# Kernel tuning notes

Hardware: AMD Instinct MI355X
Metric: run time of the kernel (lower is better)

The kernel has to match this reference:

```python
import jax, jax.numpy as jnp
import numpy as np
import math

D_MODEL = 64
D_STATE = 16
V_RANGE = 1
K = 3
BATCH, H, W = 4, 32, 32
V_LIST = [(x, y) for x in range(-V_RANGE, V_RANGE + 1) for y in range(-V_RANGE, V_RANGE + 1)]
NUM_V = len(V_LIST)


def _circ_conv(x, w):
    # x: (B, Cin, H, W), w: (Cout, Cin, K, K); circular padding then VALID conv
    p = K // 2
    xp = jnp.pad(x, ((0, 0), (0, 0), (p, p), (p, p)), mode='wrap')
    return jax.lax.conv_general_dilated(
        xp, w, window_strides=(1, 1), padding='VALID',
        dimension_numbers=('NCHW', 'OIHW', 'NCHW'))


def setup_inputs() -> dict:
    key = jax.random.key(0)
    ks = jax.random.split(key, 8)
    fan = 1.0 / math.sqrt(D_MODEL * K * K)
    u_t = jax.random.normal(ks[0], (BATCH, D_MODEL, H, W), dtype=jnp.float32)
    s_prev = jax.random.normal(ks[1], (BATCH, NUM_V, D_MODEL, D_STATE, H, W), dtype=jnp.float32)
    conv_delta_w = jax.random.normal(ks[2], (D_MODEL, D_MODEL, K, K), dtype=jnp.float32) * fan
    conv_delta_b = jax.random.normal(ks[3], (D_MODEL,), dtype=jnp.float32) * 0.01
    conv_B_w = jax.random.normal(ks[4], (D_STATE, D_MODEL, K, K), dtype=jnp.float32) * fan
    conv_C_w = jax.random.normal(ks[5], (D_STATE, D_MODEL, K, K), dtype=jnp.float32) * fan
    log_A_real = jnp.log(0.5 * jnp.ones((D_MODEL, D_STATE), dtype=jnp.float32))
    D = jnp.ones((D_MODEL,), dtype=jnp.float32)
    dt_inv_softplus = jnp.asarray(math.log(math.e - 1.0), dtype=jnp.float32)
    return {
        'u_t': u_t, 's_prev': s_prev,
        'conv_delta_w': conv_delta_w, 'conv_delta_b': conv_delta_b,
        'conv_B_w': conv_B_w, 'conv_C_w': conv_C_w,
        'log_A_real': log_A_real, 'D': D, 'dt_inv_softplus': dt_inv_softplus,
    }


def reference(u_t, s_prev, conv_delta_w, conv_delta_b, conv_B_w, conv_C_w,
              log_A_real, D, dt_inv_softplus):
    # delta: (B, d_model, h, w)
    delta = jax.nn.softplus(_circ_conv(u_t, conv_delta_w)
                            + conv_delta_b[None, :, None, None] + dt_inv_softplus)
    B_val = _circ_conv(u_t, conv_B_w)   # (B, d_state, h, w)
    C_val = _circ_conv(u_t, conv_C_w)   # (B, d_state, h, w)
    A = -jnp.exp(log_A_real)            # (d_model, d_state)
    A_bc = A[None, :, :, None, None]    # (1, d_model, d_state, 1, 1)
    A_bar = jnp.exp(delta[:, :, None] * A_bc)        # (B, d_model, d_state, h, w)
    B_bar = (A_bar - 1.0) / A_bc * B_val[:, None]    # (B, d_model, d_state, h, w)
    u_bc = u_t[:, :, None]              # (B, d_model, 1, h, w)
    C_bc = C_val[:, None]               # (B, 1, d_state, h, w)
    y_skip = u_t * D[None, :, None, None]

    s_next_list, y_list = [], []
    for i, (vx, vy) in enumerate(V_LIST):
        s_tr = jnp.roll(s_prev[:, i], shift=(-vy, -vx), axis=(-2, -1))
        s_new = A_bar * s_tr + B_bar * u_bc          # (B, d_model, d_state, h, w)
        y_new = jnp.sum(s_new * C_bc, axis=2) + y_skip
        s_next_list.append(s_new)
        y_list.append(y_new)
    s_next = jnp.stack(s_next_list, axis=1)  # (B, num_v, d_model, d_state, h, w)
    y_out = jnp.stack(y_list, axis=1)        # (B, num_v, d_model, h, w)
    return (y_out, s_next)
```

## Files before the change

kernel.cpp:

```cpp
#include <hip/hip_runtime.h>
#include <math.h>

#define NBATCH 4
#define NV 9
#define DM 64
#define DS 16

__device__ __forceinline__ float softplus_f(float x) {
    return (x > 20.f) ? x : log1pf(__expf(x));
}

__global__ void prep_kernel(const float* __restrict__ logA, float2* __restrict__ Atab) {
    int t = threadIdx.x;
    float A = -__expf(logA[t]);
    Atab[t] = make_float2(A, __builtin_amdgcn_rcpf(A));
}

__global__ __launch_bounds__(256) void conv_kernel(
    const float* __restrict__ u, const float* __restrict__ wd,
    const float* __restrict__ bd, const float* __restrict__ wb,
    const float* __restrict__ wc, const float* __restrict__ dtp,
    float* __restrict__ delta_out, float* __restrict__ Bv_out,
    float* __restrict__ Cv_out)
{
    int bx = blockIdx.x;
    int ht = bx & 3;
    int co = (bx >> 2) % 96;
    int b  = bx / 384;
    int tid = threadIdx.x;
    int chunk = __builtin_amdgcn_readfirstlane(tid >> 6);
    int pxt = tid & 63;
    int row = ht * 8 + (pxt >> 3);
    int w0  = (pxt & 7) << 2;

    const float* wbase = (co < 64) ? (wd + (size_t)co * 576)
                       : (co < 80) ? (wb + (size_t)(co - 64) * 576)
                                   : (wc + (size_t)(co - 80) * 576);

    int hm = (row + 31) & 31, hp = (row + 1) & 31;
    int wl = (w0 + 31) & 31;
    int wr = (w0 + 4) & 31;
    const float* ub = u + (size_t)b * 65536 + (size_t)(chunk << 4) * 1024;
    const float* wq0 = wbase + (size_t)(chunk << 4) * 9;

    float a0 = 0.f, a1 = 0.f, a2 = 0.f, a3 = 0.f;
    #pragma unroll 4
    for (int j = 0; j < 16; ++j) {
        const float* base = ub + j * 1024;
        const float* wq = wq0 + j * 9;
        #pragma unroll
        for (int r = 0; r < 3; ++r) {
            int rr = (r == 0) ? hm : (r == 1) ? row : hp;
            const float* rp = base + rr * 32;
            float4 v = *(const float4*)(rp + w0);
            float L = rp[wl], R = rp[wr];
            float k0 = wq[r * 3 + 0], k1 = wq[r * 3 + 1], k2 = wq[r * 3 + 2];
            a0 = fmaf(k0, L,   fmaf(k1, v.x, fmaf(k2, v.y, a0)));
            a1 = fmaf(k0, v.x, fmaf(k1, v.y, fmaf(k2, v.z, a1)));
            a2 = fmaf(k0, v.y, fmaf(k1, v.z, fmaf(k2, v.w, a2)));
            a3 = fmaf(k0, v.z, fmaf(k1, v.w, fmaf(k2, R,   a3)));
        }
    }

    __shared__ float4 part[4][64];
    part[chunk][pxt] = make_float4(a0, a1, a2, a3);
    __syncthreads();

    if (tid < 64) {
        float4 p0 = part[0][tid], p1 = part[1][tid];
        float4 p2 = part[2][tid], p3 = part[3][tid];
        float s0 = p0.x + p1.x + p2.x + p3.x;
        float s1 = p0.y + p1.y + p2.y + p3.y;
        float s2 = p0.z + p1.z + p2.z + p3.z;
        float s3 = p0.w + p1.w + p2.w + p3.w;
        int prow = ht * 8 + (tid >> 3);
        int pw   = (tid & 7) << 2;
        int pix  = prow * 32 + pw;
        if (co < 64) {
            float bias = bd[co] + dtp[0];
            float4 o;
            o.x = softplus_f(s0 + bias);
            o.y = softplus_f(s1 + bias);
            o.z = softplus_f(s2 + bias);
            o.w = softplus_f(s3 + bias);
            *(float4*)(delta_out + (((size_t)b * 64 + co) << 10) + pix) = o;
        } else if (co < 80) {
            *(float4*)(Bv_out + (((size_t)b * 16 + (co - 64)) << 10) + pix) =
                make_float4(s0, s1, s2, s3);
        } else {
            *(float4*)(Cv_out + (((size_t)b * 16 + (co - 80)) << 10) + pix) =
                make_float4(s0, s1, s2, s3);
        }
    }
}

__global__ __launch_bounds__(256) void scan_kernel(
    const float* __restrict__ u, const float* __restrict__ s_prev,
    const float2* __restrict__ Atab, const float* __restrict__ Dp,
    const float* __restrict__ delta_in, const float* __restrict__ Bv,
    const float* __restrict__ Cv,
    float* __restrict__ y_out, float* __restrict__ s_next)
{
    int bx = blockIdx.x;
    int t  = bx & 3;
    int c  = (bx >> 2) & 63;
    int bi9 = bx >> 8;
    int i  = bi9 % 9;
    int b  = bi9 / 9;

    int tid = threadIdx.x;
    int pix = (t << 8) + tid;
    int h = pix >> 5, w = pix & 31;

    int vx = i / 3 - 1;
    int vy = i % 3 - 1;
    int hh = (h + vy + 32) & 31;
    int ww = (w + vx + 32) & 31;

    size_t ub = (((size_t)b * 64 + c) << 10) + pix;
    float uv = u[ub];
    float dv = delta_in[ub];
    float y  = uv * Dp[c];

    size_t chan = (((size_t)bi9 * 64 + c) << 4);
    const float* sp  = s_prev + (chan << 10) + hh * 32 + ww;
    float*       sn  = s_next + (chan << 10) + pix;
    const float* bvp = Bv + (((size_t)b << 14)) + pix;
    const float* cvp = Cv + (((size_t)b << 14)) + pix;
    const float2* at = Atab + (c << 4);

    #pragma unroll
    for (int n = 0; n < 16; ++n) {
        float2 Ar = at[n];
        float s  = sp[n << 10];
        float bval = bvp[n << 10];
        float cval = cvp[n << 10];
        float ab = __expf(dv * Ar.x);
        float bu = (ab - 1.f) * Ar.y * bval * uv;
        float v  = fmaf(ab, s, bu);
        __builtin_nontemporal_store(v, sn + (n << 10));
        y = fmaf(v, cval, y);
    }
    __builtin_nontemporal_store(y, y_out + (((size_t)bi9 * 64 + c) << 10) + pix);
}

extern "C" void kernel_launch(void* const* d_in, const int* in_sizes, int n_in,
                              void* d_out, int out_size, void* d_ws, size_t ws_size,
                              hipStream_t stream) {
    const float* u      = (const float*)d_in[0];
    const float* s_prev = (const float*)d_in[1];
    const float* wd     = (const float*)d_in[2];
    const float* bd     = (const float*)d_in[3];
    const float* wb     = (const float*)d_in[4];
    const float* wc     = (const float*)d_in[5];
    const float* logA   = (const float*)d_in[6];
    const float* Dp     = (const float*)d_in[7];
    const float* dtp    = (const float*)d_in[8];

    float* ws    = (float*)d_ws;
    float* delta = ws;
    float* Bv    = ws + 262144;
    float* Cv    = ws + 327680;
    float2* Atab = (float2*)(ws + 393216);

    float* y_out  = (float*)d_out;
    float* s_next = y_out + (size_t)NBATCH * NV * DM * 1024;

    prep_kernel<<<dim3(1), dim3(1024), 0, stream>>>(logA, Atab);
    conv_kernel<<<dim3(4 * 96 * 4), dim3(256), 0, stream>>>(
        u, wd, bd, wb, wc, dtp, delta, Bv, Cv);
    scan_kernel<<<dim3(4 * 9 * 64 * 4), dim3(256), 0, stream>>>(
        u, s_prev, Atab, Dp, delta, Bv, Cv, y_out, s_next);
}
```

Before: 105.9 us.

## Stage s_prev channel in LDS via async loads and process four pixels per thread

```diff
diff --git a/kernel.cpp b/kernel.cpp
--- a/kernel.cpp
+++ b/kernel.cpp
@@ -6,8 +6,16 @@
 #define DM 64
 #define DS 16
 
+typedef float f32x4 __attribute__((ext_vector_type(4)));
+
 __device__ __forceinline__ float softplus_f(float x) {
     return (x > 20.f) ? x : log1pf(__expf(x));
+}
+
+__device__ __forceinline__ void gload_lds16(const float* g, float* l) {
+    __builtin_amdgcn_global_load_lds(
+        (const __attribute__((address_space(1))) void*)g,
+        (__attribute__((address_space(3))) void*)l, 16, 0, 0);
 }
 
 __global__ void prep_kernel(const float* __restrict__ logA, float2* __restrict__ Atab) {
@@ -101,47 +109,87 @@
     const float* __restrict__ Cv,
     float* __restrict__ y_out, float* __restrict__ s_next)
 {
+    __shared__ float lds[16][1024];
+
     int bx = blockIdx.x;
-    int t  = bx & 3;
-    int c  = (bx >> 2) & 63;
-    int bi9 = bx >> 8;
-    int i  = bi9 % 9;
-    int b  = bi9 / 9;
+    int c  = bx & 63;
+    int bi = bx >> 6;
+    int i  = bi % 9;
+    int b  = bi / 9;
 
     int tid = threadIdx.x;
-    int pix = (t << 8) + tid;
-    int h = pix >> 5, w = pix & 31;
-
+    int wv = tid >> 6;
+    int ln = tid & 63;
+
+    const float* gsrc = s_prev + ((size_t)(bi * 64 + c) << 14);
+    #pragma unroll
+    for (int k = 0; k < 16; ++k) {
+        gload_lds16(gsrc + (k << 10) + (wv << 8) + (ln << 2),
+                    &lds[k][wv << 8]);
+    }
+
+    int pix0 = tid << 2;
+    int h  = pix0 >> 5;
+    int w0 = pix0 & 31;
     int vx = i / 3 - 1;
     int vy = i % 3 - 1;
     int hh = (h + vy + 32) & 31;
-    int ww = (w + vx + 32) & 31;
-
-    size_t ub = (((size_t)b * 64 + c) << 10) + pix;
-    float uv = u[ub];
-    float dv = delta_in[ub];
-    float y  = uv * Dp[c];
-
-    size_t chan = (((size_t)bi9 * 64 + c) << 4);
-    const float* sp  = s_prev + (chan << 10) + hh * 32 + ww;
-    float*       sn  = s_next + (chan << 10) + pix;
-    const float* bvp = Bv + (((size_t)b << 14)) + pix;
-    const float* cvp = Cv + (((size_t)b << 14)) + pix;
-    const float2* at = Atab + (c << 4);
+
+    size_t ub = (((size_t)b * 64 + c) << 10) + pix0;
+    f32x4 u4 = *(const f32x4*)(u + ub);
+    f32x4 d4 = *(const f32x4*)(delta_in + ub);
+    float dk = Dp[c];
+    f32x4 y4 = u4 * dk;
+
+    const float2* at  = Atab + (c << 4);
+    const float*  bvp = Bv + ((size_t)b << 14) + pix0;
+    const float*  cvp = Cv + ((size_t)b << 14) + pix0;
+    float*        snb = s_next + ((size_t)(bi * 64 + c) << 14) + pix0;
+
+    __syncthreads();
+
+    int wL = (w0 + 31) & 31;
+    int wR = (w0 + 4) & 31;
 
     #pragma unroll
     for (int n = 0; n < 16; ++n) {
         float2 Ar = at[n];
-        float s  = sp[n << 10];
-        float bval = bvp[n << 10];
-        float cval = cvp[n << 10];
-        float ab = __expf(dv * Ar.x);
-        float bu = (ab - 1.f) * Ar.y * bval * uv;
-        float v  = fmaf(ab, s, bu);
-        __builtin_nontemporal_store(v, sn + (n << 10));
-        y = fmaf(v, cval, y);
-    }
-    __builtin_nontemporal_store(y, y_out + (((size_t)bi9 * 64 + c) << 10) + pix);
+        f32x4 b4 = *(const f32x4*)(bvp + (n << 10));
+        f32x4 c4 = *(const f32x4*)(cvp + (n << 10));
+
+        const float* base = &lds[n][hh << 5];
+        f32x4 v = *(const f32x4*)(base + w0);
+        float L = base[wL], R = base[wR];
+
+        float s0, s1, s2, s3;
+        if (vx == 0)      { s0 = v.x; s1 = v.y; s2 = v.z; s3 = v.w; }
+        else if (vx > 0)  { s0 = v.y; s1 = v.z; s2 = v.w; s3 = R; }
+        else              { s0 = L;   s1 = v.x; s2 = v.y; s3 = v.z; }
+
+        float e0 = __expf(d4.x * Ar.x);
+        float e1 = __expf(d4.y * Ar.x);
+        float e2 = __expf(d4.z * Ar.x);
+        float e3 = __expf(d4.w * Ar.x);
+
+        float bu0 = (e0 - 1.f) * Ar.y * b4.x * u4.x;
+        float bu1 = (e1 - 1.f) * Ar.y * b4.y * u4.y;
+        float bu2 = (e2 - 1.f) * Ar.y * b4.z * u4.z;
+        float bu3 = (e3 - 1.f) * Ar.y * b4.w * u4.w;
+
+        f32x4 sn;
+        sn.x = fmaf(e0, s0, bu0);
+        sn.y = fmaf(e1, s1, bu1);
+        sn.z = fmaf(e2, s2, bu2);
+        sn.w = fmaf(e3, s3, bu3);
+        __builtin_nontemporal_store(sn, (f32x4*)(snb + (n << 10)));
+
+        y4.x = fmaf(sn.x, c4.x, y4.x);
+        y4.y = fmaf(sn.y, c4.y, y4.y);
+        y4.z = fmaf(sn.z, c4.z, y4.z);
+        y4.w = fmaf(sn.w, c4.w, y4.w);
+    }
+    __builtin_nontemporal_store(y4,
+        (f32x4*)(y_out + (((size_t)(bi * 64 + c)) << 10) + pix0));
 }
 
 extern "C" void kernel_launch(void* const* d_in, const int* in_sizes, int n_in,
@@ -169,6 +217,6 @@
     prep_kernel<<<dim3(1), dim3(1024), 0, stream>>>(logA, Atab);
     conv_kernel<<<dim3(4 * 96 * 4), dim3(256), 0, stream>>>(
         u, wd, bd, wb, wc, dtp, delta, Bv, Cv);
-    scan_kernel<<<dim3(4 * 9 * 64 * 4), dim3(256), 0, stream>>>(
+    scan_kernel<<<dim3(36 * 64), dim3(256), 0, stream>>>(
         u, s_prev, Atab, Dp, delta, Bv, Cv, y_out, s_next);
 }
```

Measured after the change: 113.2 us. +6.9%, slower.
